# Optimization experiments

Measured on AMD Instinct MI355X. Metric: run time of the kernel, lower is better.

Reference implementation:

```python
import jax, jax.numpy as jnp
import numpy as np

V = 100000   # char_size
E = 256      # embedding_dim
H = 512      # hidden_dim
Hh = H // 2  # per-direction hidden
L = 20       # label_size
T = 4096     # sequence length
START = 18
STOP = 19
NEG = -10000.0


def setup_inputs() -> dict:
    key = jax.random.key(0)
    ks = jax.random.split(key, 16)
    s = 0.05
    x = jax.random.randint(ks[0], (1, T), 0, V, dtype=jnp.int32)
    emb = jax.random.normal(ks[1], (V, E), jnp.float32) * s
    w_ih_f = jax.random.normal(ks[2], (4 * Hh, E), jnp.float32) * s
    w_hh_f = jax.random.normal(ks[3], (4 * Hh, Hh), jnp.float32) * s
    b_ih_f = jax.random.normal(ks[4], (4 * Hh,), jnp.float32) * s
    b_hh_f = jax.random.normal(ks[5], (4 * Hh,), jnp.float32) * s
    w_ih_b = jax.random.normal(ks[6], (4 * Hh, E), jnp.float32) * s
    w_hh_b = jax.random.normal(ks[7], (4 * Hh, Hh), jnp.float32) * s
    b_ih_b = jax.random.normal(ks[8], (4 * Hh,), jnp.float32) * s
    b_hh_b = jax.random.normal(ks[9], (4 * Hh,), jnp.float32) * s
    w_out = jax.random.normal(ks[10], (L, H), jnp.float32) * s
    b_out = jax.random.normal(ks[11], (L,), jnp.float32) * s
    transitions = jax.random.normal(ks[12], (L, L), jnp.float32)
    transitions = transitions.at[START, :].set(NEG).at[:, STOP].set(NEG)
    h0 = jax.random.normal(ks[13], (2, Hh), jnp.float32)  # [direction, Hh], batch=1
    c0 = jax.random.normal(ks[14], (2, Hh), jnp.float32)
    return {"x": x, "emb": emb,
            "w_ih_f": w_ih_f, "w_hh_f": w_hh_f, "b_ih_f": b_ih_f, "b_hh_f": b_hh_f,
            "w_ih_b": w_ih_b, "w_hh_b": w_hh_b, "b_ih_b": b_ih_b, "b_hh_b": b_hh_b,
            "w_out": w_out, "b_out": b_out, "transitions": transitions,
            "h0": h0, "c0": c0}


def _lstm_dir(xs, w_ih, w_hh, b_ih, b_hh, h0, c0, reverse):
    # xs: [T, E]; PyTorch gate order i, f, g, o
    def step(carry, x_t):
        h, c = carry
        z = x_t @ w_ih.T + b_ih + h @ w_hh.T + b_hh  # [4*Hh]
        i, f, g, o = jnp.split(z, 4)
        i = jax.nn.sigmoid(i); f = jax.nn.sigmoid(f); o = jax.nn.sigmoid(o)
        g = jnp.tanh(g)
        c = f * c + i * g
        h = o * jnp.tanh(c)
        return (h, c), h
    _, hs = jax.lax.scan(step, (h0, c0), xs, reverse=reverse)
    return hs  # [T, Hh]


def _viterbi(feats, transitions):
    # feats: [T, L]; transitions[to, from]
    alpha0 = jnp.full((L,), NEG, feats.dtype).at[START].set(0.0)
    trT = transitions.T  # [from, to]
    def step(alpha, frame):
        smat = alpha[:, None] + frame[None, :] + trT  # [from, to]
        return jnp.max(smat, axis=0), jnp.argmax(smat, axis=0)
    alpha, bptrs = jax.lax.scan(step, alpha0, feats)  # bptrs: [T, L]
    final = alpha + transitions[STOP, :]
    score = jnp.max(final)
    best_last = jnp.argmax(final)
    def back(tag, bp):
        prev = bp[tag]
        return prev, prev
    _, prevs = jax.lax.scan(back, best_last, bptrs[1:], reverse=True)  # [T-1]
    path = jnp.concatenate([prevs, best_last[None]])  # [T]
    return score, path


def reference(x, emb, w_ih_f, w_hh_f, b_ih_f, b_hh_f, w_ih_b, w_hh_b, b_ih_b, b_hh_b,
              w_out, b_out, transitions, h0, c0):
    xs = emb[x[0]]  # [T, E], batch = 1
    h_f = _lstm_dir(xs, w_ih_f, w_hh_f, b_ih_f, b_hh_f, h0[0], c0[0], reverse=False)
    h_b = _lstm_dir(xs, w_ih_b, w_hh_b, b_ih_b, b_hh_b, h0[1], c0[1], reverse=True)
    lstm_out = jnp.concatenate([h_f, h_b], axis=-1)  # [T, H]
    feats = lstm_out @ w_out.T + b_out  # [T, L]
    score, path = _viterbi(feats, transitions)
    return score, path
```

## Files before the change

### kernel.cpp

```cpp
#include <hip/hip_runtime.h>
#include <hip/hip_bf16.h>
#include <stdint.h>

#define TT 4096
#define EE 256
#define LL 20
#define STARTT 18
#define STOPP 19
#define NEGV -10000.0f
#define NCH 256

typedef short v8s __attribute__((ext_vector_type(8)));
typedef float v4f __attribute__((ext_vector_type(4)));
typedef int   v4i __attribute__((ext_vector_type(4)));

__device__ inline float bf2f(unsigned short u){
  unsigned int x = ((unsigned int)u) << 16;
  return __builtin_bit_cast(float, x);
}
__device__ inline unsigned short f2bf(float f){
  unsigned int x = __builtin_bit_cast(unsigned int, f);
  unsigned int r = (x + 0x7FFFu + ((x >> 16) & 1u)) >> 16;
  return (unsigned short)r;
}

#define BARRIER_LDS() asm volatile("s_waitcnt lgkmcnt(0)\ns_barrier" ::: "memory")

constexpr size_t OFF_U    = 0;
constexpr size_t SZ_U     = 2ull*TT*1024*2;
constexpr size_t OFF_X    = OFF_U + SZ_U;
constexpr size_t SZ_X     = (size_t)TT*EE*2;
constexpr size_t OFF_WIH  = OFF_X + SZ_X;
constexpr size_t SZ_WIH   = 2048ull*256*2;
constexpr size_t OFF_BIAS = OFF_WIH + SZ_WIH;
constexpr size_t SZ_BIAS  = 2048ull*4;
constexpr size_t OFF_WQ   = OFF_BIAS + SZ_BIAS;
constexpr size_t SZ_WQ    = 2ull*8*8*4*64*16;
constexpr size_t OFF_FS   = OFF_WQ + SZ_WQ;
constexpr size_t SZ_FS    = 2ull*256*16;
constexpr size_t OFF_WOP  = OFF_FS + SZ_FS;
constexpr size_t SZ_WOP   = 32ull*512*2;
constexpr size_t OFF_HOUT = OFF_WOP + SZ_WOP;
constexpr size_t SZ_HOUT  = (size_t)TT*512*2;
constexpr size_t OFF_FE   = OFF_HOUT + SZ_HOUT;
constexpr size_t SZ_FE    = (size_t)TT*LL*4;
constexpr size_t OFF_P    = OFF_FE + SZ_FE;
constexpr size_t SZ_P     = 256ull*400*4;
constexpr size_t OFF_BAL  = OFF_P + SZ_P;
constexpr size_t SZ_BAL   = 20736;
constexpr size_t OFF_BP   = OFF_BAL + SZ_BAL;
constexpr size_t SZ_BP    = (size_t)TT*LL;
constexpr size_t OFF_M    = OFF_BP + SZ_BP;
constexpr size_t SZ_M     = 256ull*LL;
constexpr size_t OFF_EG   = OFF_M + SZ_M + 64;


__global__ void k_gather(const int* __restrict__ x, const float* __restrict__ emb,
                         unsigned short* __restrict__ X){
  int t = blockIdx.x;
  int xt = x[t];
  const float4* src = (const float4*)(emb + (size_t)xt * EE);
  float4 v = src[threadIdx.x];
  ushort4 o;
  o.x = f2bf(v.x); o.y = f2bf(v.y); o.z = f2bf(v.z); o.w = f2bf(v.w);
  ((ushort4*)(X + (size_t)t * EE))[threadIdx.x] = o;
}

__global__ void k_wih(const float* __restrict__ wf, const float* __restrict__ wb,
                      unsigned short* __restrict__ WIH){
  int gid = blockIdx.x * 256 + threadIdx.x;
  int row = gid >> 5, c8 = gid & 31;
  const float* src = (row < 1024 ? wf + (size_t)row * EE : wb + (size_t)(row - 1024) * EE) + c8 * 8;
  unsigned short* dst = WIH + (size_t)row * 256 + c8 * 8;
#pragma unroll
  for (int i = 0; i < 8; i++) dst[i] = f2bf(src[i]);
}

__global__ void k_bias(const float* bf, const float* hf, const float* bb, const float* hb,
                       float* __restrict__ bias){
  int i = blockIdx.x * 256 + threadIdx.x;
  int r = i & 1023;
  bias[i] = (i < 1024) ? (bf[r] + hf[r]) : (bb[r] + hb[r]);
}

__global__ void k_wout(const float* __restrict__ wout, unsigned short* __restrict__ WOP){
  int gid = blockIdx.x * 256 + threadIdx.x;
  int row = gid >> 9, k = gid & 511;
  WOP[gid] = (row < LL) ? f2bf(wout[row * 512 + k]) : 0;
}

__global__ void k_whh8(const float* __restrict__ whf, const float* __restrict__ whb,
                       unsigned int* __restrict__ WQ, float* __restrict__ FS){
  int row = blockIdx.x;
  int d = row >> 10, R = row & 1023;
  int g = R >> 8, J = R & 255;
  int w = J >> 5, tp = (J >> 4) & 1, n = J & 15;
  int nt = g * 2 + tp;
  const float* W = (d ? whb : whf) + (size_t)R * 256;
  int t = threadIdx.x;
  float4 v = ((const float4*)W)[t];
  float m = fmaxf(fmaxf(fabsf(v.x), fabsf(v.y)), fmaxf(fabsf(v.z), fabsf(v.w)));
#pragma unroll
  for (int o = 32; o >= 1; o >>= 1) m = fmaxf(m, __shfl_down(m, o));
  m = __shfl(m, 0);
  float sc = (m > 0.f) ? (m / 127.f) : 1.f;
  float inv = 1.f / sc;
  int a = (int)rintf(v.x * inv), b = (int)rintf(v.y * inv);
  int c = (int)rintf(v.z * inv), e4 = (int)rintf(v.w * inv);
  unsigned int pack = ((unsigned)a & 255u) | (((unsigned)b & 255u) << 8)
                    | (((unsigned)c & 255u) << 16) | (((unsigned)e4 & 255u) << 24);
  int kt = t >> 4, q = (t >> 2) & 3, comp = t & 3;
  int lane = q * 16 + n;
  size_t widx = ((((size_t)d * 8 + w) * 8 + nt) * 4 + kt) * 64 + lane;
  WQ[widx * 4 + comp] = pack;
  if (t == 0) FS[((size_t)d * 256 + J) * 4 + g] = sc;
}

__global__ void k_gemm_u(const unsigned short* __restrict__ X,
                         const unsigned short* __restrict__ WIH,
                         const float* __restrict__ bias,
                         unsigned short* __restrict__ U){
  int wave = threadIdx.x >> 6, l = threadIdx.x & 63;
  int tile = blockIdx.x * 4 + wave;
  int mt = tile & 255, nt = tile >> 8;
  int lm = l & 15, lq = l >> 4;
  const unsigned short* Arow = X   + (size_t)(mt * 16 + lm) * 256 + lq * 8;
  const unsigned short* Brow = WIH + (size_t)(nt * 16 + lm) * 256 + lq * 8;
  v4f acc = {0.f, 0.f, 0.f, 0.f};
#pragma unroll
  for (int kb = 0; kb < 8; kb++){
    v8s a = *(const v8s*)(Arow + kb * 32);
    v8s b = *(const v8s*)(Brow + kb * 32);
    acc = __builtin_amdgcn_mfma_f32_16x16x32_bf16(a, b, acc, 0, 0, 0);
  }
  int n = nt * 16 + lm;
  int dd = n >> 10, r = n & 1023;
  int g = r >> 8, J = r & 255;
  float bi = bias[n];
#pragma unroll
  for (int r4 = 0; r4 < 4; r4++){
    int t = mt * 16 + lq * 4 + r4;
    U[(((size_t)(dd * TT + t)) * 256 + J) * 4 + g] = f2bf(acc[r4] + bi);
  }
}


#define NT8(M) M(0) M(1) M(2) M(3) M(4) M(5) M(6) M(7)

#define DECLWB(nt) v4i wb0_##nt, wb1_##nt, wb2_##nt, wb3_##nt;
#define LOADWB(nt) { wb0_##nt = WQv[base + ((nt)*4 + 0) * 64]; \
                     wb1_##nt = WQv[base + ((nt)*4 + 1) * 64]; \
                     wb2_##nt = WQv[base + ((nt)*4 + 2) * 64]; \
                     wb3_##nt = WQv[base + ((nt)*4 + 3) * 64]; }
#define DECLACC(nt) v4i acc_##nt;
#define MFA(nt) acc_##nt = __builtin_amdgcn_mfma_i32_16x16x64_i8(hA0, wb0_##nt, zero,     0, 0, 0);
#define MFB(nt) acc_##nt = __builtin_amdgcn_mfma_i32_16x16x64_i8(hA1, wb1_##nt, acc_##nt, 0, 0, 0);
#define MFC(nt) acc_##nt = __builtin_amdgcn_mfma_i32_16x16x64_i8(hA2, wb2_##nt, acc_##nt, 0, 0, 0);
#define MFD(nt) acc_##nt = __builtin_amdgcn_mfma_i32_16x16x64_i8(hA3, wb3_##nt, acc_##nt, 0, 0, 0);

__global__ void __launch_bounds__(512)
__attribute__((amdgpu_waves_per_eu(2, 2)))
k_lstm15(
    const unsigned short* __restrict__ U, const v4i* __restrict__ WQv,
    const float4* __restrict__ FS4, const float* __restrict__ h0,
    const float* __restrict__ c0, unsigned short* __restrict__ hout){
  int d = blockIdx.x;
  int tid = threadIdx.x;
  int w = tid >> 6;
  int l = tid & 63;
  int q = l >> 4;
  int n = l & 15;
  int tp = l >> 5;
  int Jsel = w * 32 + tp * 16 + n;
  bool pub = ((l & 16) == 0);

  __shared__ __align__(16) unsigned char hb[2][256];

  NT8(DECLWB)
  {
    size_t base = ((size_t)(d * 8 + w)) * 2048 + l;
    NT8(LOADWB)
  }

  float4 fsv = FS4[(size_t)d * 256 + Jsel];
  float fs8x = fsv.x * (8.f/127.f), fs1x = fsv.x * (1.f/127.f);
  float fs8y = fsv.y * (8.f/127.f), fs1y = fsv.y * (1.f/127.f);
  float fs8z = fsv.z * (8.f/127.f), fs1z = fsv.z * (1.f/127.f);
  float fs8w = fsv.w * (8.f/127.f), fs1w = fsv.w * (1.f/127.f);

  float cst = c0[d * 256 + Jsel];
  if (pub){
    float hini = h0[d * 256 + Jsel];
    hini = fminf(fmaxf(hini, -8.f), 8.f);
    hb[0][Jsel] = (unsigned char)(char)(int)rintf(hini * (127.f / 8.f));
  }

  const unsigned short* Up0 = U + (size_t)d * TT * 1024 + (size_t)Jsel * 4;
  int stp = d ? -1 : 1;
  int tA = d ? TT - 1 : 0;
  uint2 u_c = *(const uint2*)(Up0 + (size_t)tA * 1024);
  uint2 u_n = *(const uint2*)(Up0 + (size_t)(tA + stp) * 1024);

  unsigned short* hp = hout + (size_t)tA * 512 + d * 256 + Jsel;

  v4i zero = {0, 0, 0, 0};

  __syncthreads();

  for (int s = 0; s < TT; s++){
    int par = s & 1;
    int tt = d ? (TT - 1 - s) : s;

    const char* hbase = (const char*)(&hb[par][0]) + (q << 4);
    v4i hA0 = *(const v4i*)(hbase);
    v4i hA1 = *(const v4i*)(hbase + 64);
    v4i hA2 = *(const v4i*)(hbase + 128);
    v4i hA3 = *(const v4i*)(hbase + 192);

    NT8(DECLACC)
    __builtin_amdgcn_s_setprio(1);
    NT8(MFA)
    NT8(MFB)
    NT8(MFC)
    NT8(MFD)
    __builtin_amdgcn_s_setprio(0);

    bool s0 = (s == 0);
    float fx = s0 ? fs8x : fs1x;
    float fy = s0 ? fs8y : fs1y;
    float fz = s0 ? fs8z : fs1z;
    float fw = s0 ? fs8w : fs1w;
    float u_i = bf2f((unsigned short)(u_c.x & 0xffffu));
    float u_f = bf2f((unsigned short)(u_c.x >> 16));
    float u_g = bf2f((unsigned short)(u_c.y & 0xffffu));
    float u_o = bf2f((unsigned short)(u_c.y >> 16));

    u_c = u_n;
    {
      int t2 = tt + 2 * stp;
      t2 = t2 < 0 ? 0 : (t2 > TT - 1 ? TT - 1 : t2);
      u_n = *(const uint2*)(Up0 + (size_t)t2 * 1024);
    }

    int aI = tp ? acc_1[0] : acc_0[0];
    int aF = tp ? acc_3[0] : acc_2[0];
    int aG = tp ? acc_5[0] : acc_4[0];
    int aO = tp ? acc_7[0] : acc_6[0];

    float zi = fmaf((float)aI, fx, u_i);
    float zf = fmaf((float)aF, fy, u_f);
    float zg = fmaf((float)aG, fz, u_g);
    float zo = fmaf((float)aO, fw, u_o);

    float ea = __expf(-zi);
    float gi = __builtin_amdgcn_rcpf(1.f + ea);
    float eb = __expf(-zf);
    float gf = __builtin_amdgcn_rcpf(1.f + eb);
    float zc = fminf(fmaxf(zg, -20.f), 20.f);
    float ec = __expf(-2.f * zc);
    float gg = (1.f - ec) * __builtin_amdgcn_rcpf(1.f + ec);
    float ed = __expf(-zo);
    float go = __builtin_amdgcn_rcpf(1.f + ed);

    cst = fmaf(gf, cst, gi * gg);
    float cc = fminf(fmaxf(cst, -20.f), 20.f);
    float e2 = __expf(-2.f * cc);
    float th = (1.f - e2) * __builtin_amdgcn_rcpf(1.f + e2);
    float h = go * th;

    if (pub){
      int qv = (int)rintf(h * 127.f);
      hb[par ^ 1][Jsel] = (unsigned char)(char)qv;
      *hp = f2bf(h);
    }
    hp += stp * 512;

    BARRIER_LDS();
  }
}

__global__ void k_feats2(const unsigned short* __restrict__ HOUT,
                         const unsigned short* __restrict__ WOP,
                         const float* __restrict__ bout,
                         float* __restrict__ feats){
  int wave = threadIdx.x >> 6, l = threadIdx.x & 63;
  int tile = blockIdx.x * 4 + wave;
  int mt = tile & 255, nt = tile >> 8;
  int lm = l & 15, lq = l >> 4;
  const unsigned short* Arow = HOUT + (size_t)(mt * 16 + lm) * 512 + lq * 8;
  const unsigned short* Brow = WOP  + (size_t)(nt * 16 + lm) * 512 + lq * 8;
  v4f acc = {0.f, 0.f, 0.f, 0.f};
#pragma unroll
  for (int kb = 0; kb < 16; kb++){
    v8s a = *(const v8s*)(Arow + kb * 32);
    v8s b = *(const v8s*)(Brow + kb * 32);
    acc = __builtin_amdgcn_mfma_f32_16x16x32_bf16(a, b, acc, 0, 0, 0);
  }
  int n = nt * 16 + lm;
  if (n < LL){
    float bi = bout[n];
#pragma unroll
    for (int r4 = 0; r4 < 4; r4++){
      int t = mt * 16 + lq * 4 + r4;
      feats[t * LL + n] = acc[r4] + bi;
    }
  }
}

__global__ void k_vchunk(const float* __restrict__ feats, const float* __restrict__ trans,
                         float* __restrict__ P){
  int c = blockIdx.x, j = threadIdx.x;
  __shared__ float Ps[2][LL][LL];
  bool act = j < LL;
  float trow[LL];
  if (act){
#pragma unroll
    for (int i = 0; i < LL; i++) trow[i] = trans[j * LL + i];
    for (int i = 0; i < LL; i++) Ps[0][i][j] = (i == j) ? 0.f : -1e30f;
  }
  __syncthreads();
  for (int s = 0; s < 16; s++){
    int t = c * 16 + s;
    int pb = s & 1;
    if (act){
      float fj = feats[t * LL + j];
      for (int i = 0; i < LL; i++){
        float m = Ps[pb][i][0] + trow[0];
#pragma unroll
        for (int mm = 1; mm < LL; mm++) m = fmaxf(m, Ps[pb][i][mm] + trow[mm]);
        Ps[pb ^ 1][i][j] = m + fj;
      }
    }
    __syncthreads();
  }
  if (act)
    for (int i = 0; i < LL; i++) P[((size_t)c * LL + i) * LL + j] = Ps[0][i][j];
}

__global__ void k_vscan(const float* __restrict__ P, float* __restrict__ bal){
  int tid = threadIdx.x;
  bool act = tid < LL;
  __shared__ float al[LL];
  __shared__ float Pl[400];
  if (act){
    float a = (tid == STARTT) ? 0.f : NEGV;
    al[tid] = a;
    bal[tid] = a;
  }
  for (int k = tid; k < 400; k += 64) Pl[k] = P[k];
  __syncthreads();
  for (int c = 0; c < NCH; c++){
    float p0 = 0.f, p1 = 0.f, p2 = 0.f, p3 = 0.f, p4 = 0.f, p5 = 0.f, p6 = 0.f;
    if (c + 1 < NCH){
      const float* Pn = P + (size_t)(c + 1) * 400;
      p0 = Pn[tid];        p1 = Pn[tid + 64];  p2 = Pn[tid + 128];
      p3 = Pn[tid + 192];  p4 = Pn[tid + 256]; p5 = Pn[tid + 320];
      if (tid + 384 < 400) p6 = Pn[tid + 384];
    }
    float m = -1e30f;
    if (act){
      m = al[0] + Pl[tid];
#pragma unroll
      for (int i = 1; i < LL; i++) m = fmaxf(m, al[i] + Pl[i * LL + tid]);
    }
    __syncthreads();
    if (act){
      al[tid] = m;
      bal[(c + 1) * LL + tid] = m;
    }
    if (c + 1 < NCH){
      Pl[tid] = p0;        Pl[tid + 64] = p1;  Pl[tid + 128] = p2;
      Pl[tid + 192] = p3;  Pl[tid + 256] = p4; Pl[tid + 320] = p5;
      if (tid + 384 < 400) Pl[tid + 384] = p6;
    }
    __syncthreads();
  }
}

__global__ void k_vbp(const float* __restrict__ feats, const float* __restrict__ trans,
                      const float* __restrict__ bal, unsigned char* __restrict__ bp,
                      unsigned char* __restrict__ M){
  int c = blockIdx.x, j = threadIdx.x;
  bool act = j < LL;
  __shared__ float al[2][LL];
  __shared__ unsigned char bpl[16][LL];
  float trow[LL];
  if (act){
#pragma unroll
    for (int i = 0; i < LL; i++) trow[i] = trans[j * LL + i];
    al[0][j] = bal[c * LL + j];
  }
  __syncthreads();
  for (int s = 0; s < 16; s++){
    int t = c * 16 + s;
    int pb = s & 1;
    if (act){
      float m = al[pb][0] + trow[0];
      int arg = 0;
#pragma unroll
      for (int i = 1; i < LL; i++){
        float v = al[pb][i] + trow[i];
        if (v > m){ m = v; arg = i; }
      }
      bpl[s][j] = (unsigned char)arg;
      bp[(size_t)t * LL + j] = (unsigned char)arg;
      al[pb ^ 1][j] = m + feats[t * LL + j];
    }
    __syncthreads();
  }
  if (act){
    int tag = j;
    for (int s = 15; s >= 0; s--) tag = bpl[s][tag];
    M[c * LL + j] = (unsigned char)tag;
  }
}

__global__ void k_vtag(const float* __restrict__ bal, const float* __restrict__ trans,
                       const unsigned char* __restrict__ M, int* __restrict__ Eg,
                       float* __restrict__ out){
  int tid = threadIdx.x;
  __shared__ unsigned char Ml[NCH * LL];
  __shared__ float fin[LL];
  for (int k = tid; k < NCH * LL; k += 64) Ml[k] = M[k];
  if (tid < LL) fin[tid] = bal[NCH * LL + tid] + trans[STOPP * LL + tid];
  __syncthreads();
  if (tid == 0){
    float m = fin[0]; int arg = 0;
    for (int i = 1; i < LL; i++) if (fin[i] > m){ m = fin[i]; arg = i; }
    out[0] = m;
    int tag = arg;
    Eg[NCH - 1] = tag;
    for (int c = NCH - 1; c >= 1; c--){
      tag = Ml[c * LL + tag];
      Eg[c - 1] = tag;
    }
  }
}

__global__ void k_vemit(const int* __restrict__ Eg, const unsigned char* __restrict__ bp,
                        float* __restrict__ out){
  int c = threadIdx.x;
  int tag = Eg[c];
  out[1 + c * 16 + 15] = (float)tag;
  for (int s = 15; s >= 1; s--){
    tag = bp[(size_t)(c * 16 + s) * LL + tag];
    out[1 + c * 16 + s - 1] = (float)tag;
  }
}

extern "C" void kernel_launch(void* const* d_in, const int* in_sizes, int n_in,
                              void* d_out, int out_size, void* d_ws, size_t ws_size,
                              hipStream_t stream){
  (void)in_sizes; (void)n_in; (void)out_size; (void)ws_size;
  const int*   x     = (const int*)d_in[0];
  const float* emb   = (const float*)d_in[1];
  const float* wihf  = (const float*)d_in[2];
  const float* whhf  = (const float*)d_in[3];
  const float* bihf  = (const float*)d_in[4];
  const float* bhhf  = (const float*)d_in[5];
  const float* wihb  = (const float*)d_in[6];
  const float* whhb  = (const float*)d_in[7];
  const float* bihb  = (const float*)d_in[8];
  const float* bhhb  = (const float*)d_in[9];
  const float* wout  = (const float*)d_in[10];
  const float* bout  = (const float*)d_in[11];
  const float* trans = (const float*)d_in[12];
  const float* h0    = (const float*)d_in[13];
  const float* c0    = (const float*)d_in[14];
  float* out = (float*)d_out;
  char* ws = (char*)d_ws;

  unsigned short* U    = (unsigned short*)(ws + OFF_U);
  unsigned short* X    = (unsigned short*)(ws + OFF_X);
  unsigned short* WIH  = (unsigned short*)(ws + OFF_WIH);
  float*          BIAS = (float*)(ws + OFF_BIAS);
  unsigned int*   WQ   = (unsigned int*)(ws + OFF_WQ);
  float*          FS   = (float*)(ws + OFF_FS);
  unsigned short* WOP  = (unsigned short*)(ws + OFF_WOP);
  unsigned short* HOUT = (unsigned short*)(ws + OFF_HOUT);
  float*          FE   = (float*)(ws + OFF_FE);
  float*          P    = (float*)(ws + OFF_P);
  float*          BAL  = (float*)(ws + OFF_BAL);
  unsigned char*  BP   = (unsigned char*)(ws + OFF_BP);
  unsigned char*  M    = (unsigned char*)(ws + OFF_M);
  int*            EG   = (int*)(ws + OFF_EG);

  k_gather<<<TT, 64, 0, stream>>>(x, emb, X);
  k_wih<<<256, 256, 0, stream>>>(wihf, wihb, WIH);
  k_bias<<<8, 256, 0, stream>>>(bihf, bhhf, bihb, bhhb, BIAS);
  k_wout<<<64, 256, 0, stream>>>(wout, WOP);
  k_whh8<<<2048, 64, 0, stream>>>(whhf, whhb, WQ, FS);
  k_gemm_u<<<8192, 256, 0, stream>>>(X, WIH, BIAS, U);
  k_lstm15<<<2, 512, 0, stream>>>(U, (const v4i*)WQ, (const float4*)FS, h0, c0, HOUT);
  k_feats2<<<128, 256, 0, stream>>>(HOUT, WOP, bout, FE);
  k_vchunk<<<NCH, 64, 0, stream>>>(FE, trans, P);
  k_vscan<<<1, 64, 0, stream>>>(P, BAL);
  k_vbp<<<NCH, 64, 0, stream>>>(FE, trans, BAL, BP, M);
  k_vtag<<<1, 64, 0, stream>>>(BAL, trans, M, EG, out);
  k_vemit<<<1, 256, 0, stream>>>(EG, BP, out);
}
```

Baseline: 3.373 ms.

## Split LSTM recurrence across 16 waves with four gate tiles each

The recurrent LSTM kernel now runs 1024 threads (16 waves) per direction instead of 512. Each wave owns 16 hidden units and computes four 16-wide gate tiles (one per gate) rather than eight, which halves the serial MFMA chain per wave per timestep. The weight-packing kernel is relaid out to match the new wave/gate tiling, and the s_setprio hints are dropped. The cost is more waves per CU (waves_per_eu 4) and more participants in each per-step barrier, which could lengthen synchronisation on the latency-bound recurrence.

```diff
diff --git a/kernel.cpp b/kernel.cpp
--- a/kernel.cpp
+++ b/kernel.cpp
@@ -35,7 +35,7 @@
 constexpr size_t OFF_BIAS = OFF_WIH + SZ_WIH;
 constexpr size_t SZ_BIAS  = 2048ull*4;
 constexpr size_t OFF_WQ   = OFF_BIAS + SZ_BIAS;
-constexpr size_t SZ_WQ    = 2ull*8*8*4*64*16;
+constexpr size_t SZ_WQ    = 2ull*16*4*4*64*16;
 constexpr size_t OFF_FS   = OFF_WQ + SZ_WQ;
 constexpr size_t SZ_FS    = 2ull*256*16;
 constexpr size_t OFF_WOP  = OFF_FS + SZ_FS;
@@ -89,13 +89,12 @@
   WOP[gid] = (row < LL) ? f2bf(wout[row * 512 + k]) : 0;
 }
 
-__global__ void k_whh8(const float* __restrict__ whf, const float* __restrict__ whb,
-                       unsigned int* __restrict__ WQ, float* __restrict__ FS){
+__global__ void k_whh11(const float* __restrict__ whf, const float* __restrict__ whb,
+                        unsigned int* __restrict__ WQ, float* __restrict__ FS){
   int row = blockIdx.x;
   int d = row >> 10, R = row & 1023;
   int g = R >> 8, J = R & 255;
-  int w = J >> 5, tp = (J >> 4) & 1, n = J & 15;
-  int nt = g * 2 + tp;
+  int w = J >> 4, n = J & 15;
   const float* W = (d ? whb : whf) + (size_t)R * 256;
   int t = threadIdx.x;
   float4 v = ((const float4*)W)[t];
@@ -111,7 +110,7 @@
                     | (((unsigned)c & 255u) << 16) | (((unsigned)e4 & 255u) << 24);
   int kt = t >> 4, q = (t >> 2) & 3, comp = t & 3;
   int lane = q * 16 + n;
-  size_t widx = ((((size_t)d * 8 + w) * 8 + nt) * 4 + kt) * 64 + lane;
+  size_t widx = ((((size_t)d * 16 + w) * 4 + g) * 4 + kt) * 64 + lane;
   WQ[widx * 4 + comp] = pack;
   if (t == 0) FS[((size_t)d * 256 + J) * 4 + g] = sc;
 }
@@ -145,7 +144,7 @@
 }
 
 
-#define NT8(M) M(0) M(1) M(2) M(3) M(4) M(5) M(6) M(7)
+#define NT4(M) M(0) M(1) M(2) M(3)
 
 #define DECLWB(nt) v4i wb0_##nt, wb1_##nt, wb2_##nt, wb3_##nt;
 #define LOADWB(nt) { wb0_##nt = WQv[base + ((nt)*4 + 0) * 64]; \
@@ -158,9 +157,9 @@
 #define MFC(nt) acc_##nt = __builtin_amdgcn_mfma_i32_16x16x64_i8(hA2, wb2_##nt, acc_##nt, 0, 0, 0);
 #define MFD(nt) acc_##nt = __builtin_amdgcn_mfma_i32_16x16x64_i8(hA3, wb3_##nt, acc_##nt, 0, 0, 0);
 
-__global__ void __launch_bounds__(512)
-__attribute__((amdgpu_waves_per_eu(2, 2)))
-k_lstm15(
+__global__ void __launch_bounds__(1024)
+__attribute__((amdgpu_waves_per_eu(4, 4)))
+k_lstm16(
     const unsigned short* __restrict__ U, const v4i* __restrict__ WQv,
     const float4* __restrict__ FS4, const float* __restrict__ h0,
     const float* __restrict__ c0, unsigned short* __restrict__ hout){
@@ -170,16 +169,15 @@
   int l = tid & 63;
   int q = l >> 4;
   int n = l & 15;
-  int tp = l >> 5;
-  int Jsel = w * 32 + tp * 16 + n;
-  bool pub = ((l & 16) == 0);
+  int Jsel = w * 16 + n;
+  bool pub = (q == 0);
 
   __shared__ __align__(16) unsigned char hb[2][256];
 
-  NT8(DECLWB)
+  NT4(DECLWB)
   {
-    size_t base = ((size_t)(d * 8 + w)) * 2048 + l;
-    NT8(LOADWB)
+    size_t base = ((size_t)(d * 16 + w)) * 1024 + l;
+    NT4(LOADWB)
   }
 
   float4 fsv = FS4[(size_t)d * 256 + Jsel];
@@ -217,13 +215,11 @@
     v4i hA2 = *(const v4i*)(hbase + 128);
     v4i hA3 = *(const v4i*)(hbase + 192);
 
-    NT8(DECLACC)
-    __builtin_amdgcn_s_setprio(1);
-    NT8(MFA)
-    NT8(MFB)
-    NT8(MFC)
-    NT8(MFD)
-    __builtin_amdgcn_s_setprio(0);
+    NT4(DECLACC)
+    NT4(MFA)
+    NT4(MFB)
+    NT4(MFC)
+    NT4(MFD)
 
     bool s0 = (s == 0);
     float fx = s0 ? fs8x : fs1x;
@@ -242,10 +238,10 @@
       u_n = *(const uint2*)(Up0 + (size_t)t2 * 1024);
     }
 
-    int aI = tp ? acc_1[0] : acc_0[0];
-    int aF = tp ? acc_3[0] : acc_2[0];
-    int aG = tp ? acc_5[0] : acc_4[0];
-    int aO = tp ? acc_7[0] : acc_6[0];
+    int aI = acc_0[0];
+    int aF = acc_1[0];
+    int aG = acc_2[0];
+    int aO = acc_3[0];
 
     float zi = fmaf((float)aI, fx, u_i);
     float zf = fmaf((float)aF, fy, u_f);
@@ -489,9 +485,9 @@
   k_wih<<<256, 256, 0, stream>>>(wihf, wihb, WIH);
   k_bias<<<8, 256, 0, stream>>>(bihf, bhhf, bihb, bhhb, BIAS);
   k_wout<<<64, 256, 0, stream>>>(wout, WOP);
-  k_whh8<<<2048, 64, 0, stream>>>(whhf, whhb, WQ, FS);
+  k_whh11<<<2048, 64, 0, stream>>>(whhf, whhb, WQ, FS);
   k_gemm_u<<<8192, 256, 0, stream>>>(X, WIH, BIAS, U);
-  k_lstm15<<<2, 512, 0, stream>>>(U, (const v4i*)WQ, (const float4*)FS, h0, c0, HOUT);
+  k_lstm16<<<2, 1024, 0, stream>>>(U, (const v4i*)WQ, (const float4*)FS, h0, c0, HOUT);
   k_feats2<<<128, 256, 0, stream>>>(HOUT, WOP, bout, FE);
   k_vchunk<<<NCH, 64, 0, stream>>>(FE, trans, P);
   k_vscan<<<1, 64, 0, stream>>>(P, BAL);
```

After: 3.575 ms. 1.06x slower.
